# Performance work log

Hardware: AMD Instinct MI355X
Metric: run time of the kernel (lower is better)

## Reference

```python
import jax, jax.numpy as jnp
import numpy as np

N_NODES = 50000
N_EDGES = 800000
IN_DIM = 128
HID = 64
OUT_DIM = 128
N_GRAPHS = 256


def setup_inputs() -> dict:
    key = jax.random.key(0)
    ks = jax.random.split(key, 8)
    x = jax.random.normal(ks[0], (N_NODES, IN_DIM), dtype=jnp.float32)
    edge_index = jax.random.randint(ks[1], (2, N_EDGES), 0, N_NODES, dtype=jnp.int64)
    batch = jnp.sort(jax.random.randint(ks[2], (N_NODES,), 0, N_GRAPHS, dtype=jnp.int64))
    # Glorot-ish init for GCN weights, zero bias (PyG default bias=True)
    W1 = jax.random.normal(ks[3], (IN_DIM, HID), dtype=jnp.float32) / np.sqrt(IN_DIM)
    b1 = jnp.zeros((HID,), dtype=jnp.float32)
    W2 = jax.random.normal(ks[4], (HID, HID), dtype=jnp.float32) / np.sqrt(HID)
    b2 = jnp.zeros((HID,), dtype=jnp.float32)
    W3 = jax.random.normal(ks[5], (HID, OUT_DIM), dtype=jnp.float32) / np.sqrt(HID)
    b3 = jnp.zeros((OUT_DIM,), dtype=jnp.float32)
    return {"x": x, "edge_index": edge_index, "batch": batch, "num_graphs": N_GRAPHS,
            "W1": W1, "b1": b1, "W2": W2, "b2": b2, "W3": W3, "b3": b3}


def _gcn_norm(edge_index, n_nodes):
    # PyG GCNConv default: add self-loops, symmetric D^{-1/2}(A+I)D^{-1/2} norm.
    loops = jnp.arange(n_nodes, dtype=edge_index.dtype)
    src = jnp.concatenate([edge_index[0], loops])  # [E + N]
    dst = jnp.concatenate([edge_index[1], loops])
    deg = jax.ops.segment_sum(jnp.ones_like(dst, dtype=jnp.float32), dst,
                              num_segments=n_nodes)
    dinv = jnp.where(deg > 0, jax.lax.rsqrt(jnp.maximum(deg, 1.0)), 0.0)
    norm = dinv[src] * dinv[dst]  # [E + N]
    return src, dst, norm


def _gcn_conv(x, W, b, src, dst, norm, n_nodes):
    h = x @ W                                  # [N, F_out] dense GEMM
    msg = h[src] * norm[:, None]               # gather + scale  [E+N, F_out]
    agg = jax.ops.segment_sum(msg, dst, num_segments=n_nodes)
    return agg + b


def reference(x, edge_index, batch, num_graphs, W1, b1, W2, b2, W3, b3):
    n_nodes = x.shape[0]
    src, dst, norm = _gcn_norm(edge_index, n_nodes)
    h = jax.nn.gelu(_gcn_conv(x, W1, b1, src, dst, norm, n_nodes))
    h = jax.nn.gelu(_gcn_conv(h, W2, b2, src, dst, norm, n_nodes))
    h = _gcn_conv(h, W3, b3, src, dst, norm, n_nodes)
    # global_mean_pool over batch segment ids
    sums = jax.ops.segment_sum(h, batch, num_segments=num_graphs)
    counts = jax.ops.segment_sum(jnp.ones((n_nodes,), dtype=h.dtype), batch,
                                 num_segments=num_graphs)
    return sums / jnp.maximum(counts, 1.0)[:, None]
```

## Files before the change

kernel.cpp:

```cpp
#include <hip/hip_runtime.h>
#include <hip/hip_fp16.h>
#include <math.h>

#define N_NODES   50000
#define N_EDGES   800000
#define IN_DIM    128
#define HID       64
#define OUT_DIM   128
#define N_GRAPHS  256
#define MAX_DEG   64
#define PARTS     8
#define PSIZE     (N_NODES / PARTS)
#define EPB       4096
#define AGG_NPB   32

typedef _Float16 half8 __attribute__((ext_vector_type(8)));
typedef float floatx4 __attribute__((ext_vector_type(4)));


__global__ __launch_bounds__(256) void k_build(const int* __restrict__ src,
                                               const int* __restrict__ dst,
                                               int* __restrict__ deg, int* __restrict__ col) {
    int p     = blockIdx.x & (PARTS - 1);
    int chunk = blockIdx.x >> 3;
    int e0    = chunk * EPB + threadIdx.x * 16;
    if (e0 + 16 > N_EDGES) return;
    int lo = p * PSIZE, hi = lo + PSIZE;

    int dd[16], ss[16];
    const int4* d4 = (const int4*)(dst + e0);
    const int4* s4 = (const int4*)(src + e0);
#pragma unroll
    for (int j = 0; j < 4; j++) {
        int4 q = d4[j];
        dd[4 * j + 0] = q.x; dd[4 * j + 1] = q.y;
        dd[4 * j + 2] = q.z; dd[4 * j + 3] = q.w;
    }
#pragma unroll
    for (int j = 0; j < 4; j++) {
        int4 q = s4[j];
        ss[4 * j + 0] = q.x; ss[4 * j + 1] = q.y;
        ss[4 * j + 2] = q.z; ss[4 * j + 3] = q.w;
    }

    int pos[16];
#pragma unroll
    for (int j = 0; j < 16; j++) {
        pos[j] = -1;
        if (dd[j] >= lo && dd[j] < hi) pos[j] = atomicAdd(&deg[dd[j]], 1);
    }
#pragma unroll
    for (int j = 0; j < 16; j++) {
        if (pos[j] >= 0 && pos[j] < MAX_DEG)
            col[(size_t)dd[j] * MAX_DEG + pos[j]] = ss[j];
    }
}

__global__ __launch_bounds__(256) void k_prep(const int* __restrict__ deg,
                                              float* __restrict__ dinv,
                                              const float* __restrict__ W1, __half* __restrict__ Wt1,
                                              const float* __restrict__ W2, __half* __restrict__ Wt2) {
    int blk = blockIdx.x;
    if (blk < 196) {
        int n = blk * 256 + threadIdx.x;
        if (n < N_NODES) dinv[n] = rsqrtf((float)(deg[n] + 1));
    } else if (blk < 200) {
        int idx = (blk - 196) * 256 + threadIdx.x;
        int g = idx >> 6, n = idx & 63;
#pragma unroll
        for (int i = 0; i < 8; i++)
            Wt1[idx * 8 + i] = __float2half(W1[(8 * g + i) * 64 + n]);
    } else {
        int idx = (blk - 200) * 256 + threadIdx.x;
        if (idx < 512) {
            int g = idx >> 6, n = idx & 63;
#pragma unroll
            for (int i = 0; i < 8; i++)
                Wt2[idx * 8 + i] = __float2half(W2[(8 * g + i) * 64 + n]);
        }
    }
}


__global__ __launch_bounds__(256) void k_mfma1(const float* __restrict__ A,
                                               const float* __restrict__ dinv,
                                               const __half* __restrict__ Bp,
                                               __half* __restrict__ C) {
    constexpr int K = IN_DIM, S = K / 32;
    int wv   = threadIdx.x >> 6;
    int lane = threadIdx.x & 63;
    int quad = lane >> 4, l15 = lane & 15;
    int row0 = blockIdx.x * 64 + wv * 16;
    if (row0 >= N_NODES) return;

    half8 bf[S][4];
#pragma unroll
    for (int s = 0; s < S; s++)
#pragma unroll
        for (int j = 0; j < 4; j++)
            bf[s][j] = *(const half8*)(Bp + ((size_t)((4 * s + quad) * 64 + 16 * j + l15)) * 8);

    floatx4 acc[4];
#pragma unroll
    for (int j = 0; j < 4; j++) acc[j] = 0.f;

    int arow = row0 + l15;
    float dv = dinv[arow];
#pragma unroll
    for (int s = 0; s < S; s++) {
        float4 xa = *(const float4*)(A + (size_t)arow * K + 32 * s + quad * 8);
        float4 xb = *(const float4*)(A + (size_t)arow * K + 32 * s + quad * 8 + 4);
        half8 af;
        af[0] = (_Float16)(xa.x * dv); af[1] = (_Float16)(xa.y * dv);
        af[2] = (_Float16)(xa.z * dv); af[3] = (_Float16)(xa.w * dv);
        af[4] = (_Float16)(xb.x * dv); af[5] = (_Float16)(xb.y * dv);
        af[6] = (_Float16)(xb.z * dv); af[7] = (_Float16)(xb.w * dv);
#pragma unroll
        for (int j = 0; j < 4; j++)
            acc[j] = __builtin_amdgcn_mfma_f32_16x16x32_f16(af, bf[s][j], acc[j], 0, 0, 0);
    }
#pragma unroll
    for (int j = 0; j < 4; j++)
#pragma unroll
        for (int r = 0; r < 4; r++)
            C[(size_t)(row0 + quad * 4 + r) * 64 + 16 * j + l15] = __float2half(acc[j][r]);
}


__global__ __launch_bounds__(256) void k_mfma2(const __half* __restrict__ A,
                                               const __half* __restrict__ Bp,
                                               __half* __restrict__ C) {
    constexpr int K = HID, S = K / 32;
    int wv   = threadIdx.x >> 6;
    int lane = threadIdx.x & 63;
    int quad = lane >> 4, l15 = lane & 15;
    int row0 = blockIdx.x * 64 + wv * 16;
    if (row0 >= N_NODES) return;

    half8 bf[S][4];
#pragma unroll
    for (int s = 0; s < S; s++)
#pragma unroll
        for (int j = 0; j < 4; j++)
            bf[s][j] = *(const half8*)(Bp + ((size_t)((4 * s + quad) * 64 + 16 * j + l15)) * 8);

    floatx4 acc[4];
#pragma unroll
    for (int j = 0; j < 4; j++) acc[j] = 0.f;

    int arow = row0 + l15;
#pragma unroll
    for (int s = 0; s < S; s++) {
        half8 af = *(const half8*)(A + (size_t)arow * K + 32 * s + quad * 8);
#pragma unroll
        for (int j = 0; j < 4; j++)
            acc[j] = __builtin_amdgcn_mfma_f32_16x16x32_f16(af, bf[s][j], acc[j], 0, 0, 0);
    }
#pragma unroll
    for (int j = 0; j < 4; j++)
#pragma unroll
        for (int r = 0; r < 4; r++)
            C[(size_t)(row0 + quad * 4 + r) * 64 + 16 * j + l15] = __float2half(acc[j][r]);
}


__device__ __forceinline__ void add8(float* acc, uint4 v) {
    const __half2* h = (const __half2*)&v;
#pragma unroll
    for (int j = 0; j < 4; j++) {
        acc[2 * j]     += __low2float(h[j]);
        acc[2 * j + 1] += __high2float(h[j]);
    }
}

__global__ __launch_bounds__(256) void k_agg(const __half* __restrict__ T,
                                             const int* __restrict__ col,
                                             const int* __restrict__ indeg,
                                             const float* __restrict__ dinv,
                                             const float* __restrict__ b,
                                             __half* __restrict__ OUT, int mode) {
    __shared__ int cols[AGG_NPB][MAX_DEG + 1];
    __shared__ int sdeg[AGG_NPB];
    int base = blockIdx.x * AGG_NPB;

    if (threadIdx.x < AGG_NPB) {
        int g = base + threadIdx.x;
        int dg0 = (g < N_NODES) ? indeg[g] : 0;
        sdeg[threadIdx.x] = dg0 > MAX_DEG ? MAX_DEG : dg0;
    }
    __syncthreads();

    for (int idx = threadIdx.x; idx < AGG_NPB * MAX_DEG; idx += 256) {
        int r = idx >> 6, j = idx & 63;
        if (j < sdeg[r]) cols[r][j] = col[(size_t)(base + r) * MAX_DEG + j];
    }
    __syncthreads();

    int lane = threadIdx.x & 63;
    int wv   = threadIdx.x >> 6;
    int q = lane >> 3, t = lane & 7;
    int local = wv * 8 + q;
    int d = base + local;
    if (d >= N_NODES) return;

    int dg = sdeg[local];

    float acc[8];
#pragma unroll
    for (int j = 0; j < 8; j++) acc[j] = 0.f;
    add8(acc, *(const uint4*)(T + (size_t)d * HID + t * 8));

    const int* cl = cols[local];
    int i = 0;
    for (; i + 4 <= dg; i += 4) {
        int s0 = cl[i], s1 = cl[i + 1], s2 = cl[i + 2], s3 = cl[i + 3];
        uint4 v0 = *(const uint4*)(T + (size_t)s0 * HID + t * 8);
        uint4 v1 = *(const uint4*)(T + (size_t)s1 * HID + t * 8);
        uint4 v2 = *(const uint4*)(T + (size_t)s2 * HID + t * 8);
        uint4 v3 = *(const uint4*)(T + (size_t)s3 * HID + t * 8);
        add8(acc, v0); add8(acc, v1); add8(acc, v2); add8(acc, v3);
    }
    for (; i < dg; i++) {
        int s = cl[i];
        add8(acc, *(const uint4*)(T + (size_t)s * HID + t * 8));
    }

    float dv = dinv[d];
    float o[8];
#pragma unroll
    for (int j = 0; j < 8; j++) o[j] = acc[j] * dv;
    if (mode == 0) {
#pragma unroll
        for (int j = 0; j < 8; j++) {
            float v = o[j] + b[t * 8 + j];
            float u2 = 0.7978845608028654f * (v + 0.044715f * v * v * v);
            o[j] = 0.5f * v * (1.0f + tanhf(u2)) * dv;
        }
    }
    __half2 hh[4];
#pragma unroll
    for (int j = 0; j < 4; j++) hh[j] = __floats2half2_rn(o[2 * j], o[2 * j + 1]);
    *(uint4*)(OUT + (size_t)d * HID + t * 8) = *(uint4*)hh;
}


__global__ __launch_bounds__(256) void k_pool_out(const __half* __restrict__ A,
                                                  const int* __restrict__ batch,
                                                  const float* __restrict__ W3,
                                                  const float* __restrict__ b3,
                                                  float* __restrict__ out) {
    int g = blockIdx.x;
    int lo = 0, hi = N_NODES;
    while (lo < hi) { int m = (lo + hi) >> 1; if (batch[m] < g) lo = m + 1; else hi = m; }
    int lo2 = lo, hi2 = N_NODES;
    while (lo2 < hi2) { int m = (lo2 + hi2) >> 1; if (batch[m] < g + 1) lo2 = m + 1; else hi2 = m; }
    int start = lo, end = lo2;

    int lane = threadIdx.x & 63;
    int wave = threadIdx.x >> 6;
    float acc = 0.f;
    for (int n = start + wave; n < end; n += 4)
        acc += __half2float(A[(size_t)n * HID + lane]);

    __shared__ float part[4][HID];
    __shared__ float pooled[HID];
    part[wave][lane] = acc;
    __syncthreads();
    if (threadIdx.x < HID)
        pooled[threadIdx.x] = part[0][threadIdx.x] + part[1][threadIdx.x] +
                              part[2][threadIdx.x] + part[3][threadIdx.x];
    __syncthreads();

    if (threadIdx.x < OUT_DIM) {
        float cntf = (float)(end - start);
        float inv = 1.0f / fmaxf(cntf, 1.0f);
        float s = 0.f;
#pragma unroll
        for (int k = 0; k < HID; k++) s += pooled[k] * W3[k * OUT_DIM + threadIdx.x];
        out[g * OUT_DIM + threadIdx.x] = (s + cntf * b3[threadIdx.x]) * inv;
    }
}


extern "C" void kernel_launch(void* const* d_in, const int* in_sizes, int n_in,
                              void* d_out, int out_size, void* d_ws, size_t ws_size,
                              hipStream_t stream) {
    const float* x     = (const float*)d_in[0];
    const int*   ei    = (const int*)d_in[1];
    const int*   batch = (const int*)d_in[2];
    const float* W1    = (const float*)d_in[4];
    const float* b1    = (const float*)d_in[5];
    const float* W2    = (const float*)d_in[6];
    const float* b2    = (const float*)d_in[7];
    const float* W3    = (const float*)d_in[8];
    const float* b3    = (const float*)d_in[9];
    float* out = (float*)d_out;

    const int* esrc = ei;
    const int* edst = ei + N_EDGES;

    int*    deg  = (int*)d_ws;
    float*  dinv = (float*)(deg + N_NODES);
    int*    col  = (int*)(dinv + N_NODES);
    __half* t    = (__half*)(col + (size_t)N_NODES * MAX_DEG);
    __half* p    = t + (size_t)N_NODES * HID;
    __half* Wt1  = p + (size_t)N_NODES * HID;
    __half* Wt2  = Wt1 + IN_DIM * HID;

    (void)hipMemsetAsync(deg, 0, (size_t)N_NODES * 4, stream);

    const int CHUNKS = (N_EDGES + EPB - 1) / EPB;
    k_build<<<CHUNKS * PARTS, 256, 0, stream>>>(esrc, edst, deg, col);
    k_prep<<<202, 256, 0, stream>>>(deg, dinv, W1, Wt1, W2, Wt2);

    const int GB = (N_NODES + 63) / 64;
    const int AB = (N_NODES + AGG_NPB - 1) / AGG_NPB;

    k_mfma1<<<GB, 256, 0, stream>>>(x, dinv, Wt1, t);
    k_agg<<<AB, 256, 0, stream>>>(t, col, deg, dinv, b1, p, 0);
    k_mfma2<<<GB, 256, 0, stream>>>(p, Wt2, t);
    k_agg<<<AB, 256, 0, stream>>>(t, col, deg, dinv, b2, p, 0);
    k_agg<<<AB, 256, 0, stream>>>(p, col, deg, dinv, b3, t, 1);
    k_pool_out<<<N_GRAPHS, 256, 0, stream>>>(t, batch, W3, b3, out);
}
```

Baseline: 218.5 us.

## Fuse first GEMM with CSR build and defer source-degree scaling to aggregation

The first-layer GEMM no longer needs dinv, so it is merged into one launch with the edge-bucketing (CSR build) blocks. The independent GEMM and atomic-scatter work can then overlap on the GPU. The source-side D^-1/2 scaling moves into the first aggregation, which now does an extra dinv gather per neighbour. The GELU tanh is also replaced with an exp-based formula, and dinv is computed in a separate small kernel after the fused launch.

```diff
diff --git a/kernel.cpp b/kernel.cpp
--- a/kernel.cpp
+++ b/kernel.cpp
@@ -13,65 +13,23 @@
 #define PSIZE     (N_NODES / PARTS)
 #define EPB       4096
 #define AGG_NPB   32
+#define GEMM_BLKS 782
 
 typedef _Float16 half8 __attribute__((ext_vector_type(8)));
 typedef float floatx4 __attribute__((ext_vector_type(4)));
 
 
-__global__ __launch_bounds__(256) void k_build(const int* __restrict__ src,
-                                               const int* __restrict__ dst,
-                                               int* __restrict__ deg, int* __restrict__ col) {
-    int p     = blockIdx.x & (PARTS - 1);
-    int chunk = blockIdx.x >> 3;
-    int e0    = chunk * EPB + threadIdx.x * 16;
-    if (e0 + 16 > N_EDGES) return;
-    int lo = p * PSIZE, hi = lo + PSIZE;
-
-    int dd[16], ss[16];
-    const int4* d4 = (const int4*)(dst + e0);
-    const int4* s4 = (const int4*)(src + e0);
-#pragma unroll
-    for (int j = 0; j < 4; j++) {
-        int4 q = d4[j];
-        dd[4 * j + 0] = q.x; dd[4 * j + 1] = q.y;
-        dd[4 * j + 2] = q.z; dd[4 * j + 3] = q.w;
-    }
-#pragma unroll
-    for (int j = 0; j < 4; j++) {
-        int4 q = s4[j];
-        ss[4 * j + 0] = q.x; ss[4 * j + 1] = q.y;
-        ss[4 * j + 2] = q.z; ss[4 * j + 3] = q.w;
-    }
-
-    int pos[16];
-#pragma unroll
-    for (int j = 0; j < 16; j++) {
-        pos[j] = -1;
-        if (dd[j] >= lo && dd[j] < hi) pos[j] = atomicAdd(&deg[dd[j]], 1);
-    }
-#pragma unroll
-    for (int j = 0; j < 16; j++) {
-        if (pos[j] >= 0 && pos[j] < MAX_DEG)
-            col[(size_t)dd[j] * MAX_DEG + pos[j]] = ss[j];
-    }
-}
-
-__global__ __launch_bounds__(256) void k_prep(const int* __restrict__ deg,
-                                              float* __restrict__ dinv,
-                                              const float* __restrict__ W1, __half* __restrict__ Wt1,
-                                              const float* __restrict__ W2, __half* __restrict__ Wt2) {
+__global__ __launch_bounds__(256) void k_prep_w(const float* __restrict__ W1, __half* __restrict__ Wt1,
+                                                const float* __restrict__ W2, __half* __restrict__ Wt2) {
     int blk = blockIdx.x;
-    if (blk < 196) {
-        int n = blk * 256 + threadIdx.x;
-        if (n < N_NODES) dinv[n] = rsqrtf((float)(deg[n] + 1));
-    } else if (blk < 200) {
-        int idx = (blk - 196) * 256 + threadIdx.x;
+    if (blk < 4) {
+        int idx = blk * 256 + threadIdx.x;
         int g = idx >> 6, n = idx & 63;
 #pragma unroll
         for (int i = 0; i < 8; i++)
             Wt1[idx * 8 + i] = __float2half(W1[(8 * g + i) * 64 + n]);
     } else {
-        int idx = (blk - 200) * 256 + threadIdx.x;
+        int idx = (blk - 4) * 256 + threadIdx.x;
         if (idx < 512) {
             int g = idx >> 6, n = idx & 63;
 #pragma unroll
@@ -82,48 +40,94 @@
 }
 
 
-__global__ __launch_bounds__(256) void k_mfma1(const float* __restrict__ A,
-                                               const float* __restrict__ dinv,
-                                               const __half* __restrict__ Bp,
-                                               __half* __restrict__ C) {
-    constexpr int K = IN_DIM, S = K / 32;
-    int wv   = threadIdx.x >> 6;
-    int lane = threadIdx.x & 63;
-    int quad = lane >> 4, l15 = lane & 15;
-    int row0 = blockIdx.x * 64 + wv * 16;
-    if (row0 >= N_NODES) return;
-
-    half8 bf[S][4];
-#pragma unroll
-    for (int s = 0; s < S; s++)
+__global__ __launch_bounds__(256) void k_fused1(const float* __restrict__ A,
+                                                const __half* __restrict__ Bp,
+                                                __half* __restrict__ C,
+                                                const int* __restrict__ src,
+                                                const int* __restrict__ dst,
+                                                int* __restrict__ deg,
+                                                int* __restrict__ col) {
+    if (blockIdx.x < GEMM_BLKS) {
+        constexpr int K = IN_DIM, S = K / 32;
+        int wv   = threadIdx.x >> 6;
+        int lane = threadIdx.x & 63;
+        int quad = lane >> 4, l15 = lane & 15;
+        int row0 = blockIdx.x * 64 + wv * 16;
+        if (row0 >= N_NODES) return;
+
+        half8 bf[S][4];
+#pragma unroll
+        for (int s = 0; s < S; s++)
+#pragma unroll
+            for (int j = 0; j < 4; j++)
+                bf[s][j] = *(const half8*)(Bp + ((size_t)((4 * s + quad) * 64 + 16 * j + l15)) * 8);
+
+        floatx4 acc[4];
+#pragma unroll
+        for (int j = 0; j < 4; j++) acc[j] = 0.f;
+
+        int arow = row0 + l15;
+#pragma unroll
+        for (int s = 0; s < S; s++) {
+            float4 xa = *(const float4*)(A + (size_t)arow * K + 32 * s + quad * 8);
+            float4 xb = *(const float4*)(A + (size_t)arow * K + 32 * s + quad * 8 + 4);
+            half8 af;
+            af[0] = (_Float16)xa.x; af[1] = (_Float16)xa.y;
+            af[2] = (_Float16)xa.z; af[3] = (_Float16)xa.w;
+            af[4] = (_Float16)xb.x; af[5] = (_Float16)xb.y;
+            af[6] = (_Float16)xb.z; af[7] = (_Float16)xb.w;
+#pragma unroll
+            for (int j = 0; j < 4; j++)
+                acc[j] = __builtin_amdgcn_mfma_f32_16x16x32_f16(af, bf[s][j], acc[j], 0, 0, 0);
+        }
 #pragma unroll
         for (int j = 0; j < 4; j++)
-            bf[s][j] = *(const half8*)(Bp + ((size_t)((4 * s + quad) * 64 + 16 * j + l15)) * 8);
-
-    floatx4 acc[4];
-#pragma unroll
-    for (int j = 0; j < 4; j++) acc[j] = 0.f;
-
-    int arow = row0 + l15;
-    float dv = dinv[arow];
-#pragma unroll
-    for (int s = 0; s < S; s++) {
-        float4 xa = *(const float4*)(A + (size_t)arow * K + 32 * s + quad * 8);
-        float4 xb = *(const float4*)(A + (size_t)arow * K + 32 * s + quad * 8 + 4);
-        half8 af;
-        af[0] = (_Float16)(xa.x * dv); af[1] = (_Float16)(xa.y * dv);
-        af[2] = (_Float16)(xa.z * dv); af[3] = (_Float16)(xa.w * dv);
-        af[4] = (_Float16)(xb.x * dv); af[5] = (_Float16)(xb.y * dv);
-        af[6] = (_Float16)(xb.z * dv); af[7] = (_Float16)(xb.w * dv);
-#pragma unroll
-        for (int j = 0; j < 4; j++)
-            acc[j] = __builtin_amdgcn_mfma_f32_16x16x32_f16(af, bf[s][j], acc[j], 0, 0, 0);
-    }
-#pragma unroll
-    for (int j = 0; j < 4; j++)
-#pragma unroll
-        for (int r = 0; r < 4; r++)
-            C[(size_t)(row0 + quad * 4 + r) * 64 + 16 * j + l15] = __float2half(acc[j][r]);
+#pragma unroll
+            for (int r = 0; r < 4; r++)
+                C[(size_t)(row0 + quad * 4 + r) * 64 + 16 * j + l15] = __float2half(acc[j][r]);
+    } else {
+        int bid   = blockIdx.x - GEMM_BLKS;
+        int p     = bid & (PARTS - 1);
+        int chunk = bid >> 3;
+        int e0    = chunk * EPB + threadIdx.x * 16;
+        if (e0 + 16 > N_EDGES) return;
+        int lo = p * PSIZE, hi = lo + PSIZE;
+
+        int dd[16], ss[16];
+        const int4* d4 = (const int4*)(dst + e0);
+        const int4* s4 = (const int4*)(src + e0);
+#pragma unroll
+        for (int j = 0; j < 4; j++) {
+            int4 q = d4[j];
+            dd[4 * j + 0] = q.x; dd[4 * j + 1] = q.y;
+            dd[4 * j + 2] = q.z; dd[4 * j + 3] = q.w;
+        }
+#pragma unroll
+        for (int j = 0; j < 4; j++) {
+            int4 q = s4[j];
+            ss[4 * j + 0] = q.x; ss[4 * j + 1] = q.y;
+            ss[4 * j + 2] = q.z; ss[4 * j + 3] = q.w;
+        }
+
+        int pos[16];
+#pragma unroll
+        for (int j = 0; j < 16; j++) {
+            pos[j] = -1;
+            if (dd[j] >= lo && dd[j] < hi) pos[j] = atomicAdd(&deg[dd[j]], 1);
+        }
+#pragma unroll
+        for (int j = 0; j < 16; j++) {
+            if (pos[j] >= 0 && pos[j] < MAX_DEG)
+                col[(size_t)dd[j] * MAX_DEG + pos[j]] = ss[j];
+        }
+    }
+}
+
+
+__global__ __launch_bounds__(256) void k_prep2(const int* __restrict__ deg,
+                                               float* __restrict__ dinv) {
+    int n = blockIdx.x * 256 + threadIdx.x;
+    if (n < N_NODES) dinv[n] = rsqrtf((float)(deg[n] + 1));
 }
 
 
@@ -164,12 +168,12 @@
 }
 
 
-__device__ __forceinline__ void add8(float* acc, uint4 v) {
+__device__ __forceinline__ void fma8(float* acc, uint4 v, float w) {
     const __half2* h = (const __half2*)&v;
 #pragma unroll
     for (int j = 0; j < 4; j++) {
-        acc[2 * j]     += __low2float(h[j]);
-        acc[2 * j + 1] += __high2float(h[j]);
+        acc[2 * j]     += w * __low2float(h[j]);
+        acc[2 * j + 1] += w * __high2float(h[j]);
     }
 }
 
@@ -178,7 +182,8 @@
                                              const int* __restrict__ indeg,
                                              const float* __restrict__ dinv,
                                              const float* __restrict__ b,
-                                             __half* __restrict__ OUT, int mode) {
+                                             __half* __restrict__ OUT,
+                                             int mode, int scale_src) {
     __shared__ int cols[AGG_NPB][MAX_DEG + 1];
     __shared__ int sdeg[AGG_NPB];
     int base = blockIdx.x * AGG_NPB;
@@ -204,11 +209,12 @@
     if (d >= N_NODES) return;
 
     int dg = sdeg[local];
+    float dv = dinv[d];
 
     float acc[8];
 #pragma unroll
     for (int j = 0; j < 8; j++) acc[j] = 0.f;
-    add8(acc, *(const uint4*)(T + (size_t)d * HID + t * 8));
+    fma8(acc, *(const uint4*)(T + (size_t)d * HID + t * 8), scale_src ? dv : 1.0f);
 
     const int* cl = cols[local];
     int i = 0;
@@ -218,14 +224,16 @@
         uint4 v1 = *(const uint4*)(T + (size_t)s1 * HID + t * 8);
         uint4 v2 = *(const uint4*)(T + (size_t)s2 * HID + t * 8);
         uint4 v3 = *(const uint4*)(T + (size_t)s3 * HID + t * 8);
-        add8(acc, v0); add8(acc, v1); add8(acc, v2); add8(acc, v3);
+        float w0 = 1.f, w1 = 1.f, w2 = 1.f, w3 = 1.f;
+        if (scale_src) { w0 = dinv[s0]; w1 = dinv[s1]; w2 = dinv[s2]; w3 = dinv[s3]; }
+        fma8(acc, v0, w0); fma8(acc, v1, w1); fma8(acc, v2, w2); fma8(acc, v3, w3);
     }
     for (; i < dg; i++) {
         int s = cl[i];
-        add8(acc, *(const uint4*)(T + (size_t)s * HID + t * 8));
-    }
-
-    float dv = dinv[d];
+        float w = scale_src ? dinv[s] : 1.f;
+        fma8(acc, *(const uint4*)(T + (size_t)s * HID + t * 8), w);
+    }
+
     float o[8];
 #pragma unroll
     for (int j = 0; j < 8; j++) o[j] = acc[j] * dv;
@@ -234,7 +242,8 @@
         for (int j = 0; j < 8; j++) {
             float v = o[j] + b[t * 8 + j];
             float u2 = 0.7978845608028654f * (v + 0.044715f * v * v * v);
-            o[j] = 0.5f * v * (1.0f + tanhf(u2)) * dv;
+            float th = 1.0f - 2.0f / (__expf(2.0f * u2) + 1.0f);
+            o[j] = 0.5f * v * (1.0f + th) * dv;
         }
     }
     __half2 hh[4];
@@ -310,16 +319,15 @@
     (void)hipMemsetAsync(deg, 0, (size_t)N_NODES * 4, stream);
 
     const int CHUNKS = (N_EDGES + EPB - 1) / EPB;
-    k_build<<<CHUNKS * PARTS, 256, 0, stream>>>(esrc, edst, deg, col);
-    k_prep<<<202, 256, 0, stream>>>(deg, dinv, W1, Wt1, W2, Wt2);
-
-    const int GB = (N_NODES + 63) / 64;
     const int AB = (N_NODES + AGG_NPB - 1) / AGG_NPB;
 
-    k_mfma1<<<GB, 256, 0, stream>>>(x, dinv, Wt1, t);
-    k_agg<<<AB, 256, 0, stream>>>(t, col, deg, dinv, b1, p, 0);
-    k_mfma2<<<GB, 256, 0, stream>>>(p, Wt2, t);
-    k_agg<<<AB, 256, 0, stream>>>(t, col, deg, dinv, b2, p, 0);
-    k_agg<<<AB, 256, 0, stream>>>(p, col, deg, dinv, b3, t, 1);
+    k_prep_w<<<6, 256, 0, stream>>>(W1, Wt1, W2, Wt2);
+    k_fused1<<<GEMM_BLKS + CHUNKS * PARTS, 256, 0, stream>>>(x, Wt1, t, esrc, edst, deg, col);
+    k_prep2<<<196, 256, 0, stream>>>(deg, dinv);
+
+    k_agg<<<AB, 256, 0, stream>>>(t, col, deg, dinv, b1, p, 0, 1);
+    k_mfma2<<<GEMM_BLKS, 256, 0, stream>>>(p, Wt2, t);
+    k_agg<<<AB, 256, 0, stream>>>(t, col, deg, dinv, b2, p, 0, 0);
+    k_agg<<<AB, 256, 0, stream>>>(p, col, deg, dinv, b3, t, 1, 0);
     k_pool_out<<<N_GRAPHS, 256, 0, stream>>>(t, batch, W3, b3, out);
 }
```

New measurement: 219.8 us. About the same (+0.6%).
